# Kernel tuning notes

Hardware: AMD Instinct MI355X
Metric: run time of the kernel (lower is better)

Reference implementation:

```python
import jax, jax.numpy as jnp
import numpy as np

B, S = 32, 512
VOCAB = 32000
D_MODEL = 512   # embedding dim
HID = 512       # LSTMCell units
LAYERS = 2


def setup_inputs() -> dict:
    key = jax.random.key(0)
    ks = jax.random.split(key, 6)
    source = jax.random.randint(ks[0], (B, S), 0, VOCAB, dtype=jnp.int32)
    source_len = jax.random.randint(ks[1], (B,), 0, S, dtype=jnp.int32)
    emb = jax.random.normal(ks[2], (VOCAB, D_MODEL), dtype=jnp.float32) * 0.02
    # Keras LSTMCell weights: kernel [in_dim, 4*units], recurrent_kernel [units, 4*units],
    # bias [4*units]; gate order i, f, c(g), o. Layer 0 in_dim = D_MODEL == HID here,
    # so all layers stack to one array.
    scale_k = 1.0 / np.sqrt(D_MODEL)
    Wk = jax.random.normal(ks[3], (LAYERS, HID, 4 * HID), dtype=jnp.float32) * scale_k
    Wr = jax.random.normal(ks[4], (LAYERS, HID, 4 * HID), dtype=jnp.float32) * scale_k
    b = jnp.zeros((LAYERS, 4 * HID), dtype=jnp.float32)
    return {"source": source, "source_len": source_len,
            "emb": emb, "Wk": Wk, "Wr": Wr, "b": b}


def _stacked_lstm(x, Wk, Wr, b):
    # x: [B, S, D]; returns [B, S, HID]
    L = Wk.shape[0]
    Bd = x.shape[0]
    h0 = jnp.zeros((L, Bd, HID), dtype=x.dtype)
    c0 = jnp.zeros((L, Bd, HID), dtype=x.dtype)

    def step(carry, x_t):
        h, c = carry            # [L, B, HID]
        inp = x_t               # [B, D]
        hs, cs = [], []
        for l in range(L):
            z = inp @ Wk[l] + h[l] @ Wr[l] + b[l]   # [B, 4*HID]
            i_g, f_g, g_g, o_g = jnp.split(z, 4, axis=-1)
            i_g = jax.nn.sigmoid(i_g)
            f_g = jax.nn.sigmoid(f_g)
            g_g = jnp.tanh(g_g)
            o_g = jax.nn.sigmoid(o_g)
            c_new = f_g * c[l] + i_g * g_g
            h_new = o_g * jnp.tanh(c_new)
            hs.append(h_new)
            cs.append(c_new)
            inp = h_new
        return (jnp.stack(hs), jnp.stack(cs)), inp

    _, ys = jax.lax.scan(step, (h0, c0), jnp.swapaxes(x, 0, 1))  # ys: [S, B, HID]
    return jnp.swapaxes(ys, 0, 1)


def reference(source, source_len, emb, Wk, Wr, b):
    source_emb = emb[source]                    # [B, S, D_MODEL]
    output = _stacked_lstm(source_emb, Wk, Wr, b)  # [B, S, HID]
    return (output, source_emb)
```

## Files before the change

### kernel.cpp

```cpp
#include <hip/hip_runtime.h>
#include <hip/hip_bf16.h>
#include <cstddef>
#include <cstdint>

#define NB 32
#define NS 512
#define ND 512
#define NG 2048

#define H0_OFF   0
#define H1_OFF   65536
#define FLAGS_OFF 131072
#define CTRL_BYTES 135168
#define XWS_OFF  135168
#define XWS_BYTES (512u*32u*512u*2u)

typedef __attribute__((ext_vector_type(8))) short short8;
typedef __attribute__((ext_vector_type(8))) __bf16 bf16x8;
typedef __attribute__((ext_vector_type(4))) float f32x4;

static __device__ __forceinline__ unsigned short f2bf(float f) {
  __hip_bfloat16 h = __float2bfloat16(f);
  return __builtin_bit_cast(unsigned short, h);
}

static __device__ __forceinline__ short8 pack8(float4 a, float4 b) {
  short8 r;
  r[0] = (short)f2bf(a.x); r[1] = (short)f2bf(a.y);
  r[2] = (short)f2bf(a.z); r[3] = (short)f2bf(a.w);
  r[4] = (short)f2bf(b.x); r[5] = (short)f2bf(b.y);
  r[6] = (short)f2bf(b.z); r[7] = (short)f2bf(b.w);
  return r;
}

__global__ __launch_bounds__(256) void gather_f32(const int* __restrict__ src,
                                                  const float* __restrict__ emb,
                                                  float* __restrict__ out1) {
  int tid = blockIdx.x * 256 + threadIdx.x;
  int bt = tid >> 7;
  int k4 = (tid & 127) << 2;
  int s  = src[bt];
  float4 v = *reinterpret_cast<const float4*>(emb + (size_t)s * ND + k4);
  *reinterpret_cast<float4*>(out1 + (size_t)bt * ND + k4) = v;
}

__global__ __launch_bounds__(256) void gather_xfrag(const int* __restrict__ src,
                                                    const float* __restrict__ emb,
                                                    unsigned char* __restrict__ xws) {
  int tid = blockIdx.x * 256 + threadIdx.x;
  int br = tid & 15;
  int mh = (tid >> 4) & 1;
  int kt = (tid >> 5) & 15;
  int t  = tid >> 9;
  int b  = mh * 16 + br;
  int s  = src[b * NS + t];
  const float* row = emb + (size_t)s * ND + kt * 32;
  unsigned char* base = xws + ((size_t)((t * 16 + kt) * 2 + mh)) * 1024 + br * 16;
#pragma unroll
  for (int qq = 0; qq < 4; ++qq) {
    float4 v0 = *reinterpret_cast<const float4*>(row + qq * 8);
    float4 v1 = *reinterpret_cast<const float4*>(row + qq * 8 + 4);
    *reinterpret_cast<short8*>(base + qq * 256) = pack8(v0, v1);
  }
}

template<bool XWS>
__global__ __launch_bounds__(256, 1) void lstm_persist(
    const float* __restrict__ Wk, const float* __restrict__ Wr,
    const float* __restrict__ bias_g,
    const float* __restrict__ x_f32,
    const unsigned char* __restrict__ xws,
    unsigned char* ws, float* __restrict__ out0) {

  __shared__ __attribute__((aligned(16))) char smem[66048];

  const int tid   = threadIdx.x;
  const int bid   = blockIdx.x;
  const int L     = bid >> 6;
  const int slice = bid & 63;
  const int u0    = slice * 8;
  const int lane  = tid & 63;
  const int wv    = tid >> 6;
  const int m     = wv & 1;
  const int kh    = wv >> 1;

  const float* WkL = Wk + (size_t)L * 512 * NG;
  const float* WrL = Wr + (size_t)L * 512 * NG;

  short* WT = reinterpret_cast<short*>(smem);
  for (int idx = tid; idx < 1024 * 32; idx += 256) {
    int k = idx >> 5, c = idx & 31;
    int gc = (c >> 3) * 512 + u0 + (c & 7);
    float v = (k < 512) ? WkL[(size_t)k * NG + gc]
                        : WrL[(size_t)(k - 512) * NG + gc];
    WT[c * 1032 + k] = (short)f2bf(v);
  }
  __syncthreads();

  short8 Bf[2][16];
  {
    int colr = lane & 15;
    int q    = lane >> 4;
#pragma unroll
    for (int n = 0; n < 2; ++n)
#pragma unroll
      for (int kt2 = 0; kt2 < 16; ++kt2) {
        int k = (kh * 16 + kt2) * 32 + q * 8;
        Bf[n][kt2] = *reinterpret_cast<const short8*>(WT + (n * 16 + colr) * 1032 + k);
      }
  }
  __syncthreads();

  float* zbuf = reinterpret_cast<float*>(smem);
  float* blds = zbuf + 2112;
  if (tid < 32) {
    int gc = (tid >> 3) * 512 + u0 + (tid & 7);
    blds[tid] = bias_g[L * NG + gc];
  }
  __syncthreads();

  int* flags = reinterpret_cast<int*>(ws + FLAGS_OFF);
  unsigned char* h0buf = ws + H0_OFF;
  unsigned char* h1buf = ws + H1_OFF;

  const int eb = tid >> 3, eu = tid & 7;
  const int pub_off = ((u0 >> 5) * 2 + (eb >> 4)) * 1024 +
                      ((u0 & 31) >> 3) * 256 + (eb & 15) * 16 + eu * 2;

  float creg = 0.f;
  bool gaveup = false;

  for (int t = 0; t < NS; ++t) {
    short8 af[16];

    if (L == 0 && kh == 0) {
      if (XWS) {
        const unsigned char* xb = xws + ((size_t)(t * 16) * 2 + m) * 1024 + lane * 16;
#pragma unroll
        for (int kt2 = 0; kt2 < 16; ++kt2)
          af[kt2] = *reinterpret_cast<const short8*>(xb + (size_t)kt2 * 2048);
      } else {
        int bb = m * 16 + (lane & 15);
        const float* xr = x_f32 + ((size_t)bb * NS + t) * ND + (lane >> 4) * 8;
#pragma unroll
        for (int kt2 = 0; kt2 < 16; ++kt2) {
          float4 v0 = *reinterpret_cast<const float4*>(xr + kt2 * 32);
          float4 v1 = *reinterpret_cast<const float4*>(xr + kt2 * 32 + 4);
          af[kt2] = pack8(v0, v1);
        }
      }
    }

    if (wv == 0 && !gaveup) {
      int n0 = (L == 0) ? t : t + 1;
      int n1 = (L == 0) ? t - 1 : t;
      int spin = 0;
      for (;; ++spin) {
        int f0 = __hip_atomic_load(flags + lane,      __ATOMIC_RELAXED, __HIP_MEMORY_SCOPE_AGENT);
        int f1 = __hip_atomic_load(flags + 64 + lane, __ATOMIC_RELAXED, __HIP_MEMORY_SCOPE_AGENT);
        if (__all(f0 >= n0 && f1 >= n1)) break;
        if (spin > (1 << 20)) { gaveup = true; break; }
        __builtin_amdgcn_s_sleep(1);
      }
    }
    __syncthreads();

    if (!(L == 0 && kh == 0)) {
      const unsigned char* hb;
      if (L == 0)      hb = h0buf + ((t - 1) & 1) * 32768;
      else if (kh == 0) hb = h0buf + (t & 1) * 32768;
      else              hb = h1buf + ((t - 1) & 1) * 32768;
      const unsigned char* ha = hb + (size_t)m * 1024 + lane * 16;
#pragma unroll
      for (int kt2 = 0; kt2 < 16; ++kt2) {
        unsigned long long* ap = reinterpret_cast<unsigned long long*>(&af[kt2]);
        unsigned long long* p  = reinterpret_cast<unsigned long long*>(
            const_cast<unsigned char*>(ha) + (size_t)kt2 * 2048);
        ap[0] = __hip_atomic_load(p,     __ATOMIC_RELAXED, __HIP_MEMORY_SCOPE_AGENT);
        ap[1] = __hip_atomic_load(p + 1, __ATOMIC_RELAXED, __HIP_MEMORY_SCOPE_AGENT);
      }
    }

    f32x4 acc0 = {0.f, 0.f, 0.f, 0.f}, acc1 = {0.f, 0.f, 0.f, 0.f};
#pragma unroll
    for (int kt2 = 0; kt2 < 16; ++kt2) {
      bf16x8 a = __builtin_bit_cast(bf16x8, af[kt2]);
      acc0 = __builtin_amdgcn_mfma_f32_16x16x32_bf16(a, __builtin_bit_cast(bf16x8, Bf[0][kt2]), acc0, 0, 0, 0);
      acc1 = __builtin_amdgcn_mfma_f32_16x16x32_bf16(a, __builtin_bit_cast(bf16x8, Bf[1][kt2]), acc1, 0, 0, 0);
    }

    {
      int r0 = m * 16 + (lane >> 4) * 4;
      int cc = lane & 15;
      float* zp = zbuf + kh * (32 * 33);
#pragma unroll
      for (int r = 0; r < 4; ++r) {
        zp[(r0 + r) * 33 + cc]      = acc0[r];
        zp[(r0 + r) * 33 + 16 + cc] = acc1[r];
      }
    }
    __syncthreads();

    {
      float zi = zbuf[eb * 33 + eu]      + zbuf[1056 + eb * 33 + eu]      + blds[eu];
      float zf = zbuf[eb * 33 + 8 + eu]  + zbuf[1056 + eb * 33 + 8 + eu]  + blds[8 + eu];
      float zg = zbuf[eb * 33 + 16 + eu] + zbuf[1056 + eb * 33 + 16 + eu] + blds[16 + eu];
      float zo = zbuf[eb * 33 + 24 + eu] + zbuf[1056 + eb * 33 + 24 + eu] + blds[24 + eu];
      float ig = 1.f / (1.f + __expf(-zi));
      float fg = 1.f / (1.f + __expf(-zf));
      float e2 = __expf(-2.f * zg);
      float gg = (1.f - e2) / (1.f + e2);
      float og = 1.f / (1.f + __expf(-zo));
      creg = fg * creg + ig * gg;
      float ec = __expf(-2.f * creg);
      float th = (1.f - ec) / (1.f + ec);
      float hv = og * th;

      if (L == 1) out0[((size_t)eb * NS + t) * ND + u0 + eu] = hv;

      unsigned int hu = f2bf(hv);
      unsigned int hi = (unsigned int)__shfl_down((int)hu, 1);
      if ((eu & 1) == 0) {
        unsigned int packed = (hu & 0xffffu) | (hi << 16);
        unsigned char* dst = ((L == 0) ? h0buf : h1buf) + (t & 1) * 32768 + pub_off;
        __hip_atomic_store(reinterpret_cast<unsigned int*>(dst), packed,
                           __ATOMIC_RELAXED, __HIP_MEMORY_SCOPE_AGENT);
      }
    }
    __syncthreads();

    if (tid == 0)
      __hip_atomic_store(flags + L * 64 + slice, t + 1,
                         __ATOMIC_RELEASE, __HIP_MEMORY_SCOPE_AGENT);
  }
}

extern "C" void kernel_launch(void* const* d_in, const int* in_sizes, int n_in,
                              void* d_out, int out_size, void* d_ws, size_t ws_size,
                              hipStream_t stream) {
  const int*   src = (const int*)d_in[0];
  const float* emb = (const float*)d_in[2];
  const float* Wk  = (const float*)d_in[3];
  const float* Wr  = (const float*)d_in[4];
  const float* bg  = (const float*)d_in[5];

  float* out0 = (float*)d_out;
  float* out1 = out0 + (size_t)NB * NS * ND;
  unsigned char* ws = (unsigned char*)d_ws;

  gather_f32<<<8192, 256, 0, stream>>>(src, emb, out1);

  hipMemsetAsync(d_ws, 0, CTRL_BYTES, stream);

  bool xws_ok = ws_size >= (size_t)XWS_OFF + (size_t)XWS_BYTES;
  if (xws_ok) {
    gather_xfrag<<<1024, 256, 0, stream>>>(src, emb, ws + XWS_OFF);
    lstm_persist<true><<<128, 256, 0, stream>>>(Wk, Wr, bg, out1, ws + XWS_OFF, ws, out0);
  } else {
    lstm_persist<false><<<128, 256, 0, stream>>>(Wk, Wr, bg, out1, ws + XWS_OFF, ws, out0);
  }
}
```

Before: 3.481 ms.

## Make LSTM waves independent with per-wave flags, 8-slot h ring, shuffle-based gates

Reorganizes the persistent LSTM kernel so that each wave owns a 16-column output tile across the full K range, instead of splitting K between waves. This removes the LDS z reduction and all block-level __syncthreads in the time loop. Gate values are exchanged through warp shuffles, and each wave publishes its own flag, which gives finer-grained waiting. The h exchange buffer grows from double buffering to an 8-slot ring, so layer 0 can run up to 7 steps ahead of layer 1. The input-projection MFMAs for layer 0 are issued before the spin-wait so they overlap with the wait. The cost is more flags to poll per wave and a hand-written vmcnt wait with relaxed flag stores, which raises the risk of memory-ordering bugs.

Result: slower. 3.905 ms (+12.2%).

```diff
diff --git a/kernel.cpp b/kernel.cpp
--- a/kernel.cpp
+++ b/kernel.cpp
@@ -8,16 +8,18 @@
 #define ND 512
 #define NG 2048
 
+#define NSLOT 8
 #define H0_OFF   0
-#define H1_OFF   65536
-#define FLAGS_OFF 131072
-#define CTRL_BYTES 135168
-#define XWS_OFF  135168
-#define XWS_BYTES (512u*32u*512u*2u)
+#define H1_OFF   (NSLOT * 32768)
+#define FLAGS_OFF (2 * NSLOT * 32768)
+#define CTRL_BYTES (FLAGS_OFF + 2048)
+#define XWS_OFF  (1u << 20)
+#define XWS_BYTES (512u * 32u * 512u * 2u)
 
 typedef __attribute__((ext_vector_type(8))) short short8;
 typedef __attribute__((ext_vector_type(8))) __bf16 bf16x8;
 typedef __attribute__((ext_vector_type(4))) float f32x4;
+typedef unsigned long long u64t;
 
 static __device__ __forceinline__ unsigned short f2bf(float f) {
   __hip_bfloat16 h = __float2bfloat16(f);
@@ -72,7 +74,7 @@
     const unsigned char* __restrict__ xws,
     unsigned char* ws, float* __restrict__ out0) {
 
-  __shared__ __attribute__((aligned(16))) char smem[66048];
+  __shared__ __attribute__((aligned(16))) short WT[32 * 1032];
 
   const int tid   = threadIdx.x;
   const int bid   = blockIdx.x;
@@ -82,156 +84,178 @@
   const int lane  = tid & 63;
   const int wv    = tid >> 6;
   const int m     = wv & 1;
-  const int kh    = wv >> 1;
+  const int n     = wv >> 1;
 
   const float* WkL = Wk + (size_t)L * 512 * NG;
   const float* WrL = Wr + (size_t)L * 512 * NG;
 
-  short* WT = reinterpret_cast<short*>(smem);
   for (int idx = tid; idx < 1024 * 32; idx += 256) {
     int k = idx >> 5, c = idx & 31;
-    int gc = (c >> 3) * 512 + u0 + (c & 7);
+    int cc = c & 15;
+    int gc = (cc >> 2) * 512 + u0 + (c >> 4) * 4 + (cc & 3);
     float v = (k < 512) ? WkL[(size_t)k * NG + gc]
                         : WrL[(size_t)(k - 512) * NG + gc];
     WT[c * 1032 + k] = (short)f2bf(v);
   }
   __syncthreads();
 
-  short8 Bf[2][16];
+  short8 Bf[32];
   {
-    int colr = lane & 15;
-    int q    = lane >> 4;
-#pragma unroll
-    for (int n = 0; n < 2; ++n)
-#pragma unroll
-      for (int kt2 = 0; kt2 < 16; ++kt2) {
-        int k = (kh * 16 + kt2) * 32 + q * 8;
-        Bf[n][kt2] = *reinterpret_cast<const short8*>(WT + (n * 16 + colr) * 1032 + k);
-      }
-  }
-  __syncthreads();
-
-  float* zbuf = reinterpret_cast<float*>(smem);
-  float* blds = zbuf + 2112;
-  if (tid < 32) {
-    int gc = (tid >> 3) * 512 + u0 + (tid & 7);
-    blds[tid] = bias_g[L * NG + gc];
-  }
-  __syncthreads();
+    int colr = lane & 15, q = lane >> 4;
+    const short* wcol = WT + (n * 16 + colr) * 1032 + q * 8;
+#pragma unroll
+    for (int kt = 0; kt < 32; ++kt)
+      Bf[kt] = *reinterpret_cast<const short8*>(wcol + kt * 32);
+  }
+  const float bval = bias_g[L * NG + ((lane >> 2) & 3) * 512 + u0 + n * 4 + (lane & 3)];
 
   int* flags = reinterpret_cast<int*>(ws + FLAGS_OFF);
-  unsigned char* h0buf = ws + H0_OFF;
-  unsigned char* h1buf = ws + H1_OFF;
-
-  const int eb = tid >> 3, eu = tid & 7;
-  const int pub_off = ((u0 >> 5) * 2 + (eb >> 4)) * 1024 +
-                      ((u0 & 31) >> 3) * 256 + (eb & 15) * 16 + eu * 2;
-
-  float creg = 0.f;
+  unsigned char* h0r = ws + H0_OFF;
+  unsigned char* h1r = ws + H1_OFF;
+  unsigned char* myring = (L == 0) ? h0r : h1r;
+
+  const int rg = lane >> 4;
+  const int gl = (lane >> 2) & 3;
+  const int uu = lane & 3;
+  const size_t pub_off = ((size_t)(u0 >> 5) * 2 + m) * 1024 +
+                         ((u0 & 31) >> 3) * 256 + (size_t)(rg * 4 + gl) * 16 + n * 8;
+  const int fbase0 = m * 128;
+  const int fbase1 = 256 + m * 128;
+
+  float cst[4] = {0.f, 0.f, 0.f, 0.f};
   bool gaveup = false;
 
   for (int t = 0; t < NS; ++t) {
-    short8 af[16];
-
-    if (L == 0 && kh == 0) {
+    f32x4 acc[4];
+#pragma unroll
+    for (int i = 0; i < 4; ++i) acc[i] = (f32x4){0.f, 0.f, 0.f, 0.f};
+    short8 af[16], af2[16];
+
+    if (L == 0) {
       if (XWS) {
-        const unsigned char* xb = xws + ((size_t)(t * 16) * 2 + m) * 1024 + lane * 16;
-#pragma unroll
-        for (int kt2 = 0; kt2 < 16; ++kt2)
-          af[kt2] = *reinterpret_cast<const short8*>(xb + (size_t)kt2 * 2048);
+        const unsigned char* xb = xws + ((size_t)t * 32 + m) * 1024 + (size_t)lane * 16;
+#pragma unroll
+        for (int kt = 0; kt < 16; ++kt)
+          af[kt] = *reinterpret_cast<const short8*>(xb + (size_t)kt * 2048);
       } else {
         int bb = m * 16 + (lane & 15);
         const float* xr = x_f32 + ((size_t)bb * NS + t) * ND + (lane >> 4) * 8;
 #pragma unroll
-        for (int kt2 = 0; kt2 < 16; ++kt2) {
-          float4 v0 = *reinterpret_cast<const float4*>(xr + kt2 * 32);
-          float4 v1 = *reinterpret_cast<const float4*>(xr + kt2 * 32 + 4);
-          af[kt2] = pack8(v0, v1);
+        for (int kt = 0; kt < 16; ++kt) {
+          float4 v0 = *reinterpret_cast<const float4*>(xr + kt * 32);
+          float4 v1 = *reinterpret_cast<const float4*>(xr + kt * 32 + 4);
+          af[kt] = pack8(v0, v1);
         }
       }
-    }
-
-    if (wv == 0 && !gaveup) {
-      int n0 = (L == 0) ? t : t + 1;
-      int n1 = (L == 0) ? t - 1 : t;
+#pragma unroll
+      for (int kt = 0; kt < 16; ++kt)
+        acc[kt & 3] = __builtin_amdgcn_mfma_f32_16x16x32_bf16(
+            __builtin_bit_cast(bf16x8, af[kt]), __builtin_bit_cast(bf16x8, Bf[kt]),
+            acc[kt & 3], 0, 0, 0);
+    }
+
+    if (!gaveup) {
+      const int n0 = (L == 0) ? t : t + 1;
+      const int n1 = (L == 0) ? t - (NSLOT - 1) : t;
       int spin = 0;
-      for (;; ++spin) {
-        int f0 = __hip_atomic_load(flags + lane,      __ATOMIC_RELAXED, __HIP_MEMORY_SCOPE_AGENT);
-        int f1 = __hip_atomic_load(flags + 64 + lane, __ATOMIC_RELAXED, __HIP_MEMORY_SCOPE_AGENT);
-        if (__all(f0 >= n0 && f1 >= n1)) break;
-        if (spin > (1 << 20)) { gaveup = true; break; }
+      for (;;) {
+        int f0a = __hip_atomic_load(flags + fbase0 + lane,      __ATOMIC_RELAXED, __HIP_MEMORY_SCOPE_AGENT);
+        int f0b = __hip_atomic_load(flags + fbase0 + 64 + lane, __ATOMIC_RELAXED, __HIP_MEMORY_SCOPE_AGENT);
+        int f1a = __hip_atomic_load(flags + fbase1 + lane,      __ATOMIC_RELAXED, __HIP_MEMORY_SCOPE_AGENT);
+        int f1b = __hip_atomic_load(flags + fbase1 + 64 + lane, __ATOMIC_RELAXED, __HIP_MEMORY_SCOPE_AGENT);
+        if (__all(f0a >= n0 && f0b >= n0 && f1a >= n1 && f1b >= n1)) break;
+        if (++spin > (1 << 18)) { gaveup = true; break; }
         __builtin_amdgcn_s_sleep(1);
       }
     }
-    __syncthreads();
-
-    if (!(L == 0 && kh == 0)) {
-      const unsigned char* hb;
-      if (L == 0)      hb = h0buf + ((t - 1) & 1) * 32768;
-      else if (kh == 0) hb = h0buf + (t & 1) * 32768;
-      else              hb = h1buf + ((t - 1) & 1) * 32768;
-      const unsigned char* ha = hb + (size_t)m * 1024 + lane * 16;
-#pragma unroll
-      for (int kt2 = 0; kt2 < 16; ++kt2) {
-        unsigned long long* ap = reinterpret_cast<unsigned long long*>(&af[kt2]);
-        unsigned long long* p  = reinterpret_cast<unsigned long long*>(
-            const_cast<unsigned char*>(ha) + (size_t)kt2 * 2048);
+    asm volatile("" ::: "memory");
+
+    {
+      const unsigned char* hb2 = myring + (size_t)((t - 1) & (NSLOT - 1)) * 32768 +
+                                 (size_t)m * 1024 + (size_t)lane * 16;
+      if (L == 1) {
+        const unsigned char* hb1 = h0r + (size_t)(t & (NSLOT - 1)) * 32768 +
+                                   (size_t)m * 1024 + (size_t)lane * 16;
+#pragma unroll
+        for (int kt = 0; kt < 16; ++kt) {
+          u64t* ap = reinterpret_cast<u64t*>(&af[kt]);
+          const u64t* p = reinterpret_cast<const u64t*>(hb1 + (size_t)kt * 2048);
+          ap[0] = __hip_atomic_load(p,     __ATOMIC_RELAXED, __HIP_MEMORY_SCOPE_AGENT);
+          ap[1] = __hip_atomic_load(p + 1, __ATOMIC_RELAXED, __HIP_MEMORY_SCOPE_AGENT);
+        }
+      }
+#pragma unroll
+      for (int kt = 0; kt < 16; ++kt) {
+        u64t* ap = reinterpret_cast<u64t*>(&af2[kt]);
+        const u64t* p = reinterpret_cast<const u64t*>(hb2 + (size_t)kt * 2048);
         ap[0] = __hip_atomic_load(p,     __ATOMIC_RELAXED, __HIP_MEMORY_SCOPE_AGENT);
         ap[1] = __hip_atomic_load(p + 1, __ATOMIC_RELAXED, __HIP_MEMORY_SCOPE_AGENT);
       }
-    }
-
-    f32x4 acc0 = {0.f, 0.f, 0.f, 0.f}, acc1 = {0.f, 0.f, 0.f, 0.f};
-#pragma unroll
-    for (int kt2 = 0; kt2 < 16; ++kt2) {
-      bf16x8 a = __builtin_bit_cast(bf16x8, af[kt2]);
-      acc0 = __builtin_amdgcn_mfma_f32_16x16x32_bf16(a, __builtin_bit_cast(bf16x8, Bf[0][kt2]), acc0, 0, 0, 0);
-      acc1 = __builtin_amdgcn_mfma_f32_16x16x32_bf16(a, __builtin_bit_cast(bf16x8, Bf[1][kt2]), acc1, 0, 0, 0);
-    }
-
+      if (L == 1) {
+#pragma unroll
+        for (int kt = 0; kt < 16; ++kt)
+          acc[kt & 3] = __builtin_amdgcn_mfma_f32_16x16x32_bf16(
+              __builtin_bit_cast(bf16x8, af[kt]), __builtin_bit_cast(bf16x8, Bf[kt]),
+              acc[kt & 3], 0, 0, 0);
+      }
+#pragma unroll
+      for (int kt = 0; kt < 16; ++kt)
+        acc[kt & 3] = __builtin_amdgcn_mfma_f32_16x16x32_bf16(
+            __builtin_bit_cast(bf16x8, af2[kt]), __builtin_bit_cast(bf16x8, Bf[16 + kt]),
+            acc[kt & 3], 0, 0, 0);
+    }
+
+    float hv[4];
     {
-      int r0 = m * 16 + (lane >> 4) * 4;
-      int cc = lane & 15;
-      float* zp = zbuf + kh * (32 * 33);
+      const int lb = lane & ~12;
 #pragma unroll
       for (int r = 0; r < 4; ++r) {
-        zp[(r0 + r) * 33 + cc]      = acc0[r];
-        zp[(r0 + r) * 33 + 16 + cc] = acc1[r];
-      }
-    }
-    __syncthreads();
+        float z = (acc[0][r] + acc[1][r]) + (acc[2][r] + acc[3][r]) + bval;
+        float zi = __shfl(z, lb);
+        float zf = __shfl(z, lb | 4);
+        float zg = __shfl(z, lb | 8);
+        float zo = __shfl(z, lb | 12);
+        float ig = 1.f / (1.f + __expf(-zi));
+        float fg = 1.f / (1.f + __expf(-zf));
+        float e2 = __expf(-2.f * zg);
+        float gg = (1.f - e2) / (1.f + e2);
+        float og = 1.f / (1.f + __expf(-zo));
+        cst[r] = fg * cst[r] + ig * gg;
+        float ec = __expf(-2.f * cst[r]);
+        hv[r] = og * (1.f - ec) / (1.f + ec);
+      }
+    }
+
+    if (L == 1 && gl == 0) {
+      float* op = out0 + ((size_t)(m * 16 + rg * 4) * NS + t) * ND + u0 + n * 4 + uu;
+#pragma unroll
+      for (int r = 0; r < 4; ++r)
+        __builtin_nontemporal_store(hv[r], op + (size_t)r * NS * ND);
+    }
 
     {
-      float zi = zbuf[eb * 33 + eu]      + zbuf[1056 + eb * 33 + eu]      + blds[eu];
-      float zf = zbuf[eb * 33 + 8 + eu]  + zbuf[1056 + eb * 33 + 8 + eu]  + blds[8 + eu];
-      float zg = zbuf[eb * 33 + 16 + eu] + zbuf[1056 + eb * 33 + 16 + eu] + blds[16 + eu];
-      float zo = zbuf[eb * 33 + 24 + eu] + zbuf[1056 + eb * 33 + 24 + eu] + blds[24 + eu];
-      float ig = 1.f / (1.f + __expf(-zi));
-      float fg = 1.f / (1.f + __expf(-zf));
-      float e2 = __expf(-2.f * zg);
-      float gg = (1.f - e2) / (1.f + e2);
-      float og = 1.f / (1.f + __expf(-zo));
-      creg = fg * creg + ig * gg;
-      float ec = __expf(-2.f * creg);
-      float th = (1.f - ec) / (1.f + ec);
-      float hv = og * th;
-
-      if (L == 1) out0[((size_t)eb * NS + t) * ND + u0 + eu] = hv;
-
-      unsigned int hu = f2bf(hv);
-      unsigned int hi = (unsigned int)__shfl_down((int)hu, 1);
-      if ((eu & 1) == 0) {
-        unsigned int packed = (hu & 0xffffu) | (hi << 16);
-        unsigned char* dst = ((L == 0) ? h0buf : h1buf) + (t & 1) * 32768 + pub_off;
-        __hip_atomic_store(reinterpret_cast<unsigned int*>(dst), packed,
-                           __ATOMIC_RELAXED, __HIP_MEMORY_SCOPE_AGENT);
-      }
-    }
-    __syncthreads();
-
-    if (tid == 0)
-      __hip_atomic_store(flags + L * 64 + slice, t + 1,
-                         __ATOMIC_RELEASE, __HIP_MEMORY_SCOPE_AGENT);
+      float tmp = (gl == 0) ? hv[0] : (gl == 1) ? hv[1] : (gl == 2) ? hv[2] : hv[3];
+      unsigned int hb = f2bf(tmp);
+      const int lb2 = lane & ~3;
+      unsigned int p0 = (unsigned int)__shfl((int)hb, lb2);
+      unsigned int p1 = (unsigned int)__shfl((int)hb, lb2 | 1);
+      unsigned int p2 = (unsigned int)__shfl((int)hb, lb2 | 2);
+      unsigned int p3 = (unsigned int)__shfl((int)hb, lb2 | 3);
+      if (uu == 0) {
+        u64t packed = (u64t)(p0 & 0xffffu)
+                    | ((u64t)(p1 & 0xffffu) << 16)
+                    | ((u64t)(p2 & 0xffffu) << 32)
+                    | ((u64t)(p3 & 0xffffu) << 48);
+        __hip_atomic_store(reinterpret_cast<u64t*>(
+              myring + (size_t)(t & (NSLOT - 1)) * 32768 + pub_off),
+            packed, __ATOMIC_RELAXED, __HIP_MEMORY_SCOPE_AGENT);
+      }
+    }
+
+    asm volatile("s_waitcnt vmcnt(0)" ::: "memory");
+    if (lane == 0)
+      __hip_atomic_store(flags + L * 256 + m * 128 + slice * 2 + n, t + 1,
+                         __ATOMIC_RELAXED, __HIP_MEMORY_SCOPE_AGENT);
   }
 }
 
```
